# Optimization experiments

Measured on AMD Instinct MI355X. Metric: run time of the kernel, lower is better.

The kernel has to match this reference:

```python
import jax, jax.numpy as jnp
import numpy as np

B, S, D = 8, 4096, 256


def setup_inputs() -> dict:
    key = jax.random.key(0)
    kq, kk, kv, kb = jax.random.split(key, 4)
    q = jax.random.normal(kq, (B, S, D), dtype=jnp.float32)
    k = jax.random.normal(kk, (B, S, D), dtype=jnp.float32)
    v = jax.random.normal(kv, (B, S, D), dtype=jnp.float32)
    beta = jax.random.uniform(kb, (B, S), dtype=jnp.float32)
    return {"q": q, "k": k, "v": v, "beta": beta}


def reference(q, k, v, beta):
    # Delta-rule linear attention recurrence:
    #   h_t = beta_t * h_{t-1} + k_t^T v_t   (h: [B, D, D])
    #   o_t = q_t @ h_t                      (o: [B, D])
    dtype = q.dtype
    b, s, d = q.shape
    h0 = jnp.zeros((b, d, d), dtype=dtype)

    def step(h, inp):
        q_t, k_t, v_t, b_t = inp  # q_t/k_t/v_t: [B, D], b_t: [B]
        h = h * b_t[:, None, None] + jnp.einsum('bi,bj->bij', k_t, v_t)
        o_t = jnp.einsum('bi,bij->bj', q_t, h)
        return h, o_t

    xs = (q.transpose(1, 0, 2), k.transpose(1, 0, 2),
          v.transpose(1, 0, 2), beta.T)  # time-major
    _, out = jax.lax.scan(step, h0, xs)  # out: [S, B, D]
    return out.transpose(1, 0, 2)  # [B, S, D]
```

## Files before the change

### kernel.cpp

```cpp
#include <hip/hip_runtime.h>
#include <hip/hip_bf16.h>
#include <math.h>


#define B_ 8
#define S_ 4096
#define D_ 256
#define L_ 64
#define C_ (S_ / L_)
#define BC_ (B_ * C_)
#define STK 66

typedef __attribute__((ext_vector_type(8))) short s8v;
typedef __attribute__((ext_vector_type(4))) float f4v;
typedef unsigned short u16;
typedef unsigned int u32;

__device__ __forceinline__ u32 pk2(float lo, float hi) {
  union { __hip_bfloat162 h; u32 u; } cv;
  cv.h = __float22bfloat162_rn(make_float2(lo, hi));
  return cv.u;
}
__device__ __forceinline__ s8v pack8(const float4 a, const float4 b) {
  union { u32 u[4]; s8v v; } r;
  r.u[0] = pk2(a.x, a.y); r.u[1] = pk2(a.z, a.w);
  r.u[2] = pk2(b.x, b.y); r.u[3] = pk2(b.z, b.w);
  return r.v;
}

__global__ __launch_bounds__(512, 4) void ks_summary4(
    const float* __restrict__ kg, const float* __restrict__ vg,
    const float* __restrict__ beta, u16* __restrict__ A,
    float* __restrict__ P)
{
  __shared__ float ls[L_];
  __shared__ __align__(16) u16 KT[D_ * STK];
  __shared__ __align__(16) u16 VT[D_ * STK];

  const int bc = blockIdx.x;
  const int b = bc / C_, c = bc % C_;
  const int tid = threadIdx.x;
  const float* betap = beta + (size_t)b * S_ + (size_t)c * L_;
  const float* kbase = kg + ((size_t)b * S_ + (size_t)c * L_) * D_;
  const float* vbase = vg + ((size_t)b * S_ + (size_t)c * L_) * D_;

  if (tid < 64) {
    float x = log2f(fmaxf(betap[tid], 1e-30f));
#pragma unroll
    for (int off = 1; off < 64; off <<= 1) {
      float y = __shfl_up(x, off);
      if (tid >= off) x += y;
    }
    ls[tid] = x;
    if (tid == 63) P[bc] = exp2f(x);
  }
  __syncthreads();
  const float ltot = ls[63];

  {
    const int half = tid >> 8;
    const int t2 = tid & 255;
    const int iL = t2 & 7;
    const int s0 = (t2 >> 3) * 2;
    const float* src0 = (half == 0 ? kbase : vbase) + (size_t)s0 * D_;
    const float* src1 = src0 + D_;
    float w0 = 1.f, w1 = 1.f;
    if (half == 0) { w0 = exp2f(ltot - ls[s0]); w1 = exp2f(ltot - ls[s0 + 1]); }
    u16* dst = (half == 0) ? KT : VT;
#pragma unroll
    for (int p = 0; p < 8; ++p) {
      const int i0 = p * 32 + iL * 4;
      float a0[4], a1[4];
      *(float4*)a0 = *(const float4*)(src0 + i0);
      *(float4*)a1 = *(const float4*)(src1 + i0);
#pragma unroll
      for (int u = 0; u < 4; ++u)
        *(u32*)&dst[(i0 + u) * STK + s0] = pk2(a0[u] * w0, a1[u] * w1);
    }
  }
  __syncthreads();

  const int lane = tid & 63, wave = tid >> 6;
  const int quad = lane >> 4, l15 = lane & 15;
  const int i0w = wave * 32;

  s8v af[2][2];
#pragma unroll
  for (int mt = 0; mt < 2; ++mt)
#pragma unroll
    for (int ks = 0; ks < 2; ++ks)
      af[mt][ks] = *(const s8v*)&KT[(i0w + mt * 16 + l15) * STK +
                                    ks * 32 + quad * 8];
  __syncthreads();

  u16* Ab = A + (size_t)bc * D_ * D_;
  u16* BN = KT;

  for (int ng = 0; ng < 4; ++ng) {
    f4v acc[2][4];
#pragma unroll
    for (int mt = 0; mt < 2; ++mt)
#pragma unroll
      for (int nt = 0; nt < 4; ++nt) acc[mt][nt] = (f4v){0.f, 0.f, 0.f, 0.f};

#pragma unroll
    for (int ks = 0; ks < 2; ++ks) {
      const int so = ks * 32 + quad * 8;
      s8v bv[4];
#pragma unroll
      for (int nt = 0; nt < 4; ++nt)
        bv[nt] = *(const s8v*)&VT[(ng * 64 + nt * 16 + l15) * STK + so];
#pragma unroll
      for (int mt = 0; mt < 2; ++mt)
#pragma unroll
        for (int nt = 0; nt < 4; ++nt)
          acc[mt][nt] = __builtin_amdgcn_mfma_f32_16x16x32_bf16(
              af[mt][ks], bv[nt], acc[mt][nt], 0, 0, 0);
    }
#pragma unroll
    for (int mt = 0; mt < 2; ++mt)
#pragma unroll
      for (int nt = 0; nt < 4; ++nt) {
        const int jl = nt * 16 + l15;
        uint2 w;
        w.x = pk2(acc[mt][nt][0], acc[mt][nt][1]);
        w.y = pk2(acc[mt][nt][2], acc[mt][nt][3]);
        *(uint2*)&BN[jl * 264 + i0w + mt * 16 + quad * 4] = w;
      }
    __syncthreads();
    {
      const int jl = tid >> 3;
      const int il = (tid & 7) * 8;
#pragma unroll
      for (int p = 0; p < 4; ++p) {
        const int iu = il + p * 64;
        *(s8v*)&Ab[(size_t)(ng * 64 + jl) * D_ + iu] =
            *(const s8v*)&BN[jl * 264 + iu];
      }
    }
    __syncthreads();
  }
}

__global__ __launch_bounds__(256) void ks_scan4(
    u16* __restrict__ A, const float* __restrict__ P)
{
  const int g = blockIdx.x;
  const int b = g >> 7;
  const int idx = ((g & 127) << 8) + threadIdx.x;
  u16* base = A + (size_t)b * ((size_t)C_ * D_ * D_) + (size_t)idx * 2;
  const float* Pb = P + b * C_;

  float h0 = 0.f, h1 = 0.f;
  u32 cur = *(const u32*)base;
  u32 nx = *(const u32*)(base + (size_t)(D_ * D_));
  float pc = Pb[0], pn = Pb[1];
#pragma unroll 4
  for (int c = 0; c < C_; ++c) {
    u16* p = base + (size_t)c * (D_ * D_);
    u32 n2 = 0; float p2 = 0.f;
    if (c + 2 < C_) {
      n2 = *(const u32*)(p + 2 * (size_t)(D_ * D_));
      p2 = Pb[c + 2];
    }
    const float a0 = __uint_as_float(cur << 16);
    const float a1 = __uint_as_float(cur & 0xFFFF0000u);
    *(u32*)p = pk2(h0, h1);
    h0 = fmaf(pc, h0, a0);
    h1 = fmaf(pc, h1, a1);
    cur = nx; pc = pn; nx = n2; pn = p2;
  }
}

__global__ __launch_bounds__(512, 4) void ks_output4(
    const float* __restrict__ qg, const float* __restrict__ kg,
    const float* __restrict__ vg, const float* __restrict__ beta,
    const u16* __restrict__ Hg, float* __restrict__ outg)
{
  __shared__ float ls[L_];
  __shared__ float cv[L_];
  __shared__ __align__(16) u16 QB[L_ * 264];
  __shared__ __align__(16) u16 UN[L_ * 264];
  __shared__ __align__(16) u16 Tm[L_ * 72];

  const int bc = blockIdx.x;
  const int b = bc / C_, c = bc % C_;
  const int tid = threadIdx.x;
  const float* betap = beta + (size_t)b * S_ + (size_t)c * L_;
  const float* qbase = qg + ((size_t)b * S_ + (size_t)c * L_) * D_;
  const float* kbase = kg + ((size_t)b * S_ + (size_t)c * L_) * D_;
  const float* vbase = vg + ((size_t)b * S_ + (size_t)c * L_) * D_;
  const u16* Hb = Hg + (size_t)bc * D_ * D_;

  if (tid < 64) {
    float x = log2f(fmaxf(betap[tid], 1e-30f));
#pragma unroll
    for (int off = 1; off < 64; off <<= 1) {
      float y = __shfl_up(x, off);
      if (tid >= off) x += y;
    }
    ls[tid] = x;
  }

  {
    const int half = tid >> 8;
    const int t2 = tid & 255;
    const int t = t2 >> 2;
    const int cg = (t2 & 3) * 8;
    const float* src = (half == 0 ? qbase : kbase) + (size_t)t * D_ + cg;
    u16* dst = (half == 0) ? QB : UN;
#pragma unroll
    for (int p = 0; p < 8; ++p) {
      const s8v pk = pack8(*(const float4*)(src + p * 32),
                           *(const float4*)(src + p * 32 + 4));
      *(s8v*)&dst[t * 264 + cg + p * 32] = pk;
    }
  }
  __syncthreads();
  if (tid < 64) cv[tid] = exp2f(ls[tid]);

  const int lane = tid & 63, wave = tid >> 6;
  const int quad = lane >> 4, l15 = lane & 15;

  {
    const int mA = (wave & 3) * 16;
    const int nB = (wave >> 2) * 32;
    f4v accA[2];
#pragma unroll
    for (int i = 0; i < 2; ++i) accA[i] = (f4v){0.f, 0.f, 0.f, 0.f};
#pragma unroll
    for (int kd = 0; kd < 8; ++kd) {
      const int d0 = kd * 32 + quad * 8;
      const s8v af = *(const s8v*)&UN[(mA + l15) * 264 + d0];
#pragma unroll
      for (int i = 0; i < 2; ++i) {
        const s8v bf = *(const s8v*)&QB[(nB + i * 16 + l15) * 264 + d0];
        accA[i] = __builtin_amdgcn_mfma_f32_16x16x32_bf16(af, bf, accA[i],
                                                          0, 0, 0);
      }
    }
#pragma unroll
    for (int i = 0; i < 2; ++i) {
      const int t = nB + i * 16 + l15;
      const float lt = ls[t];
      const int s0 = mA + quad * 4;
      float v[4];
#pragma unroll
      for (int r = 0; r < 4; ++r) {
        const int s = s0 + r;
        v[r] = (s <= t) ? accA[i][r] * exp2f(lt - ls[s]) : 0.f;
      }
      uint2 w;
      w.x = pk2(v[0], v[1]);
      w.y = pk2(v[2], v[3]);
      *(uint2*)&Tm[t * 72 + s0] = w;
    }
  }
  __syncthreads();

  u16* VT = UN;
  {
    const int iL = tid & 15;
    const int s0 = (tid >> 4) * 2;
#pragma unroll
    for (int p = 0; p < 4; ++p) {
      const int i0 = p * 64 + iL * 4;
      float a0[4], a1[4];
      *(float4*)a0 = *(const float4*)(vbase + (size_t)s0 * D_ + i0);
      *(float4*)a1 = *(const float4*)(vbase + (size_t)(s0 + 1) * D_ + i0);
#pragma unroll
      for (int u = 0; u < 4; ++u)
        *(u32*)&VT[(i0 + u) * STK + s0] = pk2(a0[u], a1[u]);
    }
  }
  __syncthreads();

  const int j0w = wave * 32;
  f4v accS[2][4], accH[2][4];
#pragma unroll
  for (int mt = 0; mt < 2; ++mt)
#pragma unroll
    for (int nt = 0; nt < 4; ++nt) {
      accS[mt][nt] = (f4v){0.f, 0.f, 0.f, 0.f};
      accH[mt][nt] = (f4v){0.f, 0.f, 0.f, 0.f};
    }

#pragma unroll
  for (int ks = 0; ks < 2; ++ks) {
    const int so = ks * 32 + quad * 8;
    s8v af[2], bf[4];
#pragma unroll
    for (int mt = 0; mt < 2; ++mt)
      af[mt] = *(const s8v*)&VT[(j0w + mt * 16 + l15) * STK + so];
#pragma unroll
    for (int nt = 0; nt < 4; ++nt)
      bf[nt] = *(const s8v*)&Tm[(nt * 16 + l15) * 72 + so];
#pragma unroll
    for (int mt = 0; mt < 2; ++mt)
#pragma unroll
      for (int nt = 0; nt < 4; ++nt)
        accS[mt][nt] = __builtin_amdgcn_mfma_f32_16x16x32_bf16(
            af[mt], bf[nt], accS[mt][nt], 0, 0, 0);
  }

#pragma unroll
  for (int ks = 0; ks < 8; ++ks) {
    const int io = ks * 32 + quad * 8;
    s8v af[2], bf[4];
#pragma unroll
    for (int mt = 0; mt < 2; ++mt)
      af[mt] = *(const s8v*)(Hb + (size_t)(j0w + mt * 16 + l15) * D_ + io);
#pragma unroll
    for (int nt = 0; nt < 4; ++nt)
      bf[nt] = *(const s8v*)&QB[(nt * 16 + l15) * 264 + io];
#pragma unroll
    for (int mt = 0; mt < 2; ++mt)
#pragma unroll
      for (int nt = 0; nt < 4; ++nt)
        accH[mt][nt] = __builtin_amdgcn_mfma_f32_16x16x32_bf16(
            af[mt], bf[nt], accH[mt][nt], 0, 0, 0);
  }

  float* ob = outg + ((size_t)b * S_ + (size_t)c * L_) * D_;
#pragma unroll
  for (int mt = 0; mt < 2; ++mt)
#pragma unroll
    for (int nt = 0; nt < 4; ++nt) {
      const int t = nt * 16 + l15;
      const float ct = cv[t];
      const int j0 = j0w + mt * 16 + quad * 4;
      float4 o;
      o.x = accS[mt][nt][0] + ct * accH[mt][nt][0];
      o.y = accS[mt][nt][1] + ct * accH[mt][nt][1];
      o.z = accS[mt][nt][2] + ct * accH[mt][nt][2];
      o.w = accS[mt][nt][3] + ct * accH[mt][nt][3];
      *(float4*)(ob + (size_t)t * D_ + j0) = o;
    }
}

extern "C" void kernel_launch(void* const* d_in, const int* in_sizes, int n_in,
                              void* d_out, int out_size, void* d_ws,
                              size_t ws_size, hipStream_t stream) {
  const float* q = (const float*)d_in[0];
  const float* k = (const float*)d_in[1];
  const float* v = (const float*)d_in[2];
  const float* beta = (const float*)d_in[3];
  float* out = (float*)d_out;

  u16* A = (u16*)d_ws;
  float* P = (float*)((char*)d_ws + (size_t)BC_ * D_ * D_ * sizeof(u16));

  ks_summary4<<<dim3(BC_), dim3(512), 0, stream>>>(k, v, beta, A, P);
  ks_scan4<<<dim3(1024), dim3(256), 0, stream>>>(A, P);
  ks_output4<<<dim3(BC_), dim3(512), 0, stream>>>(q, k, v, beta, A, out);
}
```

Baseline: 189.7 us.

## Double chunk length to 128 to halve chunk-state traffic

```diff
diff --git a/kernel.cpp b/kernel.cpp
--- a/kernel.cpp
+++ b/kernel.cpp
@@ -6,7 +6,7 @@
 #define B_ 8
 #define S_ 4096
 #define D_ 256
-#define L_ 64
+#define L_ 128
 #define C_ (S_ / L_)
 #define BC_ (B_ * C_)
 #define STK 66
@@ -28,14 +28,35 @@
   return r.v;
 }
 
-__global__ __launch_bounds__(512, 4) void ks_summary4(
+__device__ __forceinline__ void beta_scan128(const float* betap, float* ls,
+                                             int tid) {
+  if (tid < 64) {
+    float x = log2f(fmaxf(betap[tid], 1e-30f));
+#pragma unroll
+    for (int off = 1; off < 64; off <<= 1) {
+      float y = __shfl_up(x, off);
+      if (tid >= off) x += y;
+    }
+    ls[tid] = x;
+    const float tot0 = __shfl(x, 63);
+    float z = log2f(fmaxf(betap[64 + tid], 1e-30f));
+#pragma unroll
+    for (int off = 1; off < 64; off <<= 1) {
+      float y = __shfl_up(z, off);
+      if (tid >= off) z += y;
+    }
+    ls[64 + tid] = z + tot0;
+  }
+}
+
+__global__ __launch_bounds__(512, 2) void ks_summary5(
     const float* __restrict__ kg, const float* __restrict__ vg,
     const float* __restrict__ beta, u16* __restrict__ A,
     float* __restrict__ P)
 {
   __shared__ float ls[L_];
-  __shared__ __align__(16) u16 KT[D_ * STK];
-  __shared__ __align__(16) u16 VT[D_ * STK];
+  __shared__ __align__(16) u16 U[2][256 * STK];
+  __shared__ __align__(16) u16 BN[64 * 264];
 
   const int bc = blockIdx.x;
   const int b = bc / C_, c = bc % C_;
@@ -44,38 +65,32 @@
   const float* kbase = kg + ((size_t)b * S_ + (size_t)c * L_) * D_;
   const float* vbase = vg + ((size_t)b * S_ + (size_t)c * L_) * D_;
 
-  if (tid < 64) {
-    float x = log2f(fmaxf(betap[tid], 1e-30f));
-#pragma unroll
-    for (int off = 1; off < 64; off <<= 1) {
-      float y = __shfl_up(x, off);
-      if (tid >= off) x += y;
-    }
-    ls[tid] = x;
-    if (tid == 63) P[bc] = exp2f(x);
-  }
-  __syncthreads();
-  const float ltot = ls[63];
+  beta_scan128(betap, ls, tid);
+  __syncthreads();
+  const float ltot = ls[L_ - 1];
+  if (tid == 0) P[bc] = exp2f(ltot);
+
+  const int hh = tid >> 8;
+  const int t2 = tid & 255;
+  const int iLs = t2 & 7;
+  const int s0s = (t2 >> 3) * 2;
+  const int sg = hh * 64 + s0s;
 
   {
-    const int half = tid >> 8;
-    const int t2 = tid & 255;
-    const int iL = t2 & 7;
-    const int s0 = (t2 >> 3) * 2;
-    const float* src0 = (half == 0 ? kbase : vbase) + (size_t)s0 * D_;
+    const float* src0 = kbase + (size_t)sg * D_;
     const float* src1 = src0 + D_;
-    float w0 = 1.f, w1 = 1.f;
-    if (half == 0) { w0 = exp2f(ltot - ls[s0]); w1 = exp2f(ltot - ls[s0 + 1]); }
-    u16* dst = (half == 0) ? KT : VT;
+    const float w0 = exp2f(ltot - ls[sg]);
+    const float w1 = exp2f(ltot - ls[sg + 1]);
+    u16* dst = U[hh];
 #pragma unroll
     for (int p = 0; p < 8; ++p) {
-      const int i0 = p * 32 + iL * 4;
+      const int i0 = p * 32 + iLs * 4;
       float a0[4], a1[4];
       *(float4*)a0 = *(const float4*)(src0 + i0);
       *(float4*)a1 = *(const float4*)(src1 + i0);
 #pragma unroll
       for (int u = 0; u < 4; ++u)
-        *(u32*)&dst[(i0 + u) * STK + s0] = pk2(a0[u] * w0, a1[u] * w1);
+        *(u32*)&dst[(i0 + u) * STK + s0s] = pk2(a0[u] * w0, a1[u] * w1);
     }
   }
   __syncthreads();
@@ -84,17 +99,33 @@
   const int quad = lane >> 4, l15 = lane & 15;
   const int i0w = wave * 32;
 
-  s8v af[2][2];
+  s8v af[2][4];
 #pragma unroll
   for (int mt = 0; mt < 2; ++mt)
 #pragma unroll
-    for (int ks = 0; ks < 2; ++ks)
-      af[mt][ks] = *(const s8v*)&KT[(i0w + mt * 16 + l15) * STK +
-                                    ks * 32 + quad * 8];
+    for (int ks = 0; ks < 4; ++ks)
+      af[mt][ks] = *(const s8v*)&U[ks >> 1][(i0w + mt * 16 + l15) * STK +
+                                            (ks & 1) * 32 + quad * 8];
+  __syncthreads();
+
+  {
+    const float* src0 = vbase + (size_t)sg * D_;
+    const float* src1 = src0 + D_;
+    u16* dst = U[hh];
+#pragma unroll
+    for (int p = 0; p < 8; ++p) {
+      const int i0 = p * 32 + iLs * 4;
+      float a0[4], a1[4];
+      *(float4*)a0 = *(const float4*)(src0 + i0);
+      *(float4*)a1 = *(const float4*)(src1 + i0);
+#pragma unroll
+      for (int u = 0; u < 4; ++u)
+        *(u32*)&dst[(i0 + u) * STK + s0s] = pk2(a0[u], a1[u]);
+    }
+  }
   __syncthreads();
 
   u16* Ab = A + (size_t)bc * D_ * D_;
-  u16* BN = KT;
 
   for (int ng = 0; ng < 4; ++ng) {
     f4v acc[2][4];
@@ -104,12 +135,12 @@
       for (int nt = 0; nt < 4; ++nt) acc[mt][nt] = (f4v){0.f, 0.f, 0.f, 0.f};
 
 #pragma unroll
-    for (int ks = 0; ks < 2; ++ks) {
-      const int so = ks * 32 + quad * 8;
+    for (int ks = 0; ks < 4; ++ks) {
+      const int so = (ks & 1) * 32 + quad * 8;
       s8v bv[4];
 #pragma unroll
       for (int nt = 0; nt < 4; ++nt)
-        bv[nt] = *(const s8v*)&VT[(ng * 64 + nt * 16 + l15) * STK + so];
+        bv[nt] = *(const s8v*)&U[ks >> 1][(ng * 64 + nt * 16 + l15) * STK + so];
 #pragma unroll
       for (int mt = 0; mt < 2; ++mt)
 #pragma unroll
@@ -142,7 +173,7 @@
   }
 }
 
-__global__ __launch_bounds__(256) void ks_scan4(
+__global__ __launch_bounds__(256) void ks_scan5(
     u16* __restrict__ A, const float* __restrict__ P)
 {
   const int g = blockIdx.x;
@@ -172,7 +203,7 @@
   }
 }
 
-__global__ __launch_bounds__(512, 4) void ks_output4(
+__global__ __launch_bounds__(512, 2) void ks_output5(
     const float* __restrict__ qg, const float* __restrict__ kg,
     const float* __restrict__ vg, const float* __restrict__ beta,
     const u16* __restrict__ Hg, float* __restrict__ outg)
@@ -180,8 +211,8 @@
   __shared__ float ls[L_];
   __shared__ float cv[L_];
   __shared__ __align__(16) u16 QB[L_ * 264];
-  __shared__ __align__(16) u16 UN[L_ * 264];
-  __shared__ __align__(16) u16 Tm[L_ * 72];
+  __shared__ __align__(16) u16 Tm[L_ * 136];
+  __shared__ __align__(16) u16 VT[256 * STK];
 
   const int bc = blockIdx.x;
   const int b = bc / C_, c = bc % C_;
@@ -192,148 +223,144 @@
   const float* vbase = vg + ((size_t)b * S_ + (size_t)c * L_) * D_;
   const u16* Hb = Hg + (size_t)bc * D_ * D_;
 
-  if (tid < 64) {
-    float x = log2f(fmaxf(betap[tid], 1e-30f));
-#pragma unroll
-    for (int off = 1; off < 64; off <<= 1) {
-      float y = __shfl_up(x, off);
-      if (tid >= off) x += y;
-    }
-    ls[tid] = x;
-  }
+  beta_scan128(betap, ls, tid);
 
   {
-    const int half = tid >> 8;
-    const int t2 = tid & 255;
-    const int t = t2 >> 2;
-    const int cg = (t2 & 3) * 8;
-    const float* src = (half == 0 ? qbase : kbase) + (size_t)t * D_ + cg;
-    u16* dst = (half == 0) ? QB : UN;
+    const int t = tid >> 2;
+    const int cg = (tid & 3) * 8;
+    const float* src = qbase + (size_t)t * D_ + cg;
 #pragma unroll
     for (int p = 0; p < 8; ++p) {
       const s8v pk = pack8(*(const float4*)(src + p * 32),
                            *(const float4*)(src + p * 32 + 4));
-      *(s8v*)&dst[t * 264 + cg + p * 32] = pk;
-    }
-  }
-  __syncthreads();
-  if (tid < 64) cv[tid] = exp2f(ls[tid]);
+      *(s8v*)&QB[t * 264 + cg + p * 32] = pk;
+    }
+  }
+  __syncthreads();
+  if (tid < L_) cv[tid] = exp2f(ls[tid]);
 
   const int lane = tid & 63, wave = tid >> 6;
   const int quad = lane >> 4, l15 = lane & 15;
 
   {
-    const int mA = (wave & 3) * 16;
-    const int nB = (wave >> 2) * 32;
-    f4v accA[2];
-#pragma unroll
-    for (int i = 0; i < 2; ++i) accA[i] = (f4v){0.f, 0.f, 0.f, 0.f};
+    const int mA = wave * 16;
+    f4v accA[8];
+#pragma unroll
+    for (int i = 0; i < 8; ++i) accA[i] = (f4v){0.f, 0.f, 0.f, 0.f};
 #pragma unroll
     for (int kd = 0; kd < 8; ++kd) {
       const int d0 = kd * 32 + quad * 8;
-      const s8v af = *(const s8v*)&UN[(mA + l15) * 264 + d0];
-#pragma unroll
-      for (int i = 0; i < 2; ++i) {
-        const s8v bf = *(const s8v*)&QB[(nB + i * 16 + l15) * 264 + d0];
-        accA[i] = __builtin_amdgcn_mfma_f32_16x16x32_bf16(af, bf, accA[i],
-                                                          0, 0, 0);
-      }
-    }
-#pragma unroll
-    for (int i = 0; i < 2; ++i) {
-      const int t = nB + i * 16 + l15;
+      const float* krow = kbase + (size_t)(mA + l15) * D_ + d0;
+      const s8v af = pack8(*(const float4*)krow, *(const float4*)(krow + 4));
+#pragma unroll
+      for (int nt = 0; nt < 8; ++nt) {
+        const s8v bf = *(const s8v*)&QB[(nt * 16 + l15) * 264 + d0];
+        accA[nt] = __builtin_amdgcn_mfma_f32_16x16x32_bf16(af, bf, accA[nt],
+                                                           0, 0, 0);
+      }
+    }
+#pragma unroll
+    for (int nt = 0; nt < 8; ++nt) {
+      const int t = nt * 16 + l15;
       const float lt = ls[t];
       const int s0 = mA + quad * 4;
       float v[4];
 #pragma unroll
       for (int r = 0; r < 4; ++r) {
         const int s = s0 + r;
-        v[r] = (s <= t) ? accA[i][r] * exp2f(lt - ls[s]) : 0.f;
+        v[r] = (s <= t) ? accA[nt][r] * exp2f(lt - ls[s]) : 0.f;
       }
       uint2 w;
       w.x = pk2(v[0], v[1]);
       w.y = pk2(v[2], v[3]);
-      *(uint2*)&Tm[t * 72 + s0] = w;
-    }
-  }
-  __syncthreads();
-
-  u16* VT = UN;
-  {
-    const int iL = tid & 15;
-    const int s0 = (tid >> 4) * 2;
-#pragma unroll
-    for (int p = 0; p < 4; ++p) {
-      const int i0 = p * 64 + iL * 4;
-      float a0[4], a1[4];
-      *(float4*)a0 = *(const float4*)(vbase + (size_t)s0 * D_ + i0);
-      *(float4*)a1 = *(const float4*)(vbase + (size_t)(s0 + 1) * D_ + i0);
-#pragma unroll
-      for (int u = 0; u < 4; ++u)
-        *(u32*)&VT[(i0 + u) * STK + s0] = pk2(a0[u], a1[u]);
+      *(uint2*)&Tm[t * 136 + s0] = w;
     }
   }
   __syncthreads();
 
   const int j0w = wave * 32;
-  f4v accS[2][4], accH[2][4];
+  f4v acc[2][8];
 #pragma unroll
   for (int mt = 0; mt < 2; ++mt)
 #pragma unroll
-    for (int nt = 0; nt < 4; ++nt) {
-      accS[mt][nt] = (f4v){0.f, 0.f, 0.f, 0.f};
-      accH[mt][nt] = (f4v){0.f, 0.f, 0.f, 0.f};
-    }
-
-#pragma unroll
-  for (int ks = 0; ks < 2; ++ks) {
-    const int so = ks * 32 + quad * 8;
-    s8v af[2], bf[4];
-#pragma unroll
-    for (int mt = 0; mt < 2; ++mt)
-      af[mt] = *(const s8v*)&VT[(j0w + mt * 16 + l15) * STK + so];
-#pragma unroll
-    for (int nt = 0; nt < 4; ++nt)
-      bf[nt] = *(const s8v*)&Tm[(nt * 16 + l15) * 72 + so];
-#pragma unroll
-    for (int mt = 0; mt < 2; ++mt)
-#pragma unroll
-      for (int nt = 0; nt < 4; ++nt)
-        accS[mt][nt] = __builtin_amdgcn_mfma_f32_16x16x32_bf16(
-            af[mt], bf[nt], accS[mt][nt], 0, 0, 0);
-  }
+    for (int nt = 0; nt < 8; ++nt) acc[mt][nt] = (f4v){0.f, 0.f, 0.f, 0.f};
 
 #pragma unroll
   for (int ks = 0; ks < 8; ++ks) {
     const int io = ks * 32 + quad * 8;
-    s8v af[2], bf[4];
+    s8v af[2], bf[8];
 #pragma unroll
     for (int mt = 0; mt < 2; ++mt)
       af[mt] = *(const s8v*)(Hb + (size_t)(j0w + mt * 16 + l15) * D_ + io);
 #pragma unroll
-    for (int nt = 0; nt < 4; ++nt)
+    for (int nt = 0; nt < 8; ++nt)
       bf[nt] = *(const s8v*)&QB[(nt * 16 + l15) * 264 + io];
 #pragma unroll
     for (int mt = 0; mt < 2; ++mt)
 #pragma unroll
-      for (int nt = 0; nt < 4; ++nt)
-        accH[mt][nt] = __builtin_amdgcn_mfma_f32_16x16x32_bf16(
-            af[mt], bf[nt], accH[mt][nt], 0, 0, 0);
+      for (int nt = 0; nt < 8; ++nt)
+        acc[mt][nt] = __builtin_amdgcn_mfma_f32_16x16x32_bf16(
+            af[mt], bf[nt], acc[mt][nt], 0, 0, 0);
+  }
+#pragma unroll
+  for (int nt = 0; nt < 8; ++nt) {
+    const float ct = cv[nt * 16 + l15];
+#pragma unroll
+    for (int mt = 0; mt < 2; ++mt) {
+      acc[mt][nt][0] *= ct; acc[mt][nt][1] *= ct;
+      acc[mt][nt][2] *= ct; acc[mt][nt][3] *= ct;
+    }
+  }
+
+#pragma unroll
+  for (int h = 0; h < 2; ++h) {
+    __syncthreads();
+    {
+      const int iL = tid & 15;
+      const int s0 = ((tid >> 4) & 31) * 2;
+      const float* src0 = vbase + (size_t)(h * 64 + s0) * D_;
+      const float* src1 = src0 + D_;
+#pragma unroll
+      for (int p = 0; p < 4; ++p) {
+        const int i0 = p * 64 + iL * 4;
+        float a0[4], a1[4];
+        *(float4*)a0 = *(const float4*)(src0 + i0);
+        *(float4*)a1 = *(const float4*)(src1 + i0);
+#pragma unroll
+        for (int u = 0; u < 4; ++u)
+          *(u32*)&VT[(i0 + u) * STK + s0] = pk2(a0[u], a1[u]);
+      }
+    }
+    __syncthreads();
+#pragma unroll
+    for (int ks = 0; ks < 2; ++ks) {
+      const int so = ks * 32 + quad * 8;
+      s8v af[2], bf[8];
+#pragma unroll
+      for (int mt = 0; mt < 2; ++mt)
+        af[mt] = *(const s8v*)&VT[(j0w + mt * 16 + l15) * STK + so];
+#pragma unroll
+      for (int nt = 0; nt < 8; ++nt)
+        bf[nt] = *(const s8v*)&Tm[(nt * 16 + l15) * 136 + h * 64 + so];
+#pragma unroll
+      for (int mt = 0; mt < 2; ++mt)
+#pragma unroll
+        for (int nt = 0; nt < 8; ++nt)
+          acc[mt][nt] = __builtin_amdgcn_mfma_f32_16x16x32_bf16(
+              af[mt], bf[nt], acc[mt][nt], 0, 0, 0);
+    }
   }
 
   float* ob = outg + ((size_t)b * S_ + (size_t)c * L_) * D_;
 #pragma unroll
   for (int mt = 0; mt < 2; ++mt)
 #pragma unroll
-    for (int nt = 0; nt < 4; ++nt) {
+    for (int nt = 0; nt < 8; ++nt) {
       const int t = nt * 16 + l15;
-      const float ct = cv[t];
       const int j0 = j0w + mt * 16 + quad * 4;
       float4 o;
-      o.x = accS[mt][nt][0] + ct * accH[mt][nt][0];
-      o.y = accS[mt][nt][1] + ct * accH[mt][nt][1];
-      o.z = accS[mt][nt][2] + ct * accH[mt][nt][2];
-      o.w = accS[mt][nt][3] + ct * accH[mt][nt][3];
+      o.x = acc[mt][nt][0]; o.y = acc[mt][nt][1];
+      o.z = acc[mt][nt][2]; o.w = acc[mt][nt][3];
       *(float4*)(ob + (size_t)t * D_ + j0) = o;
     }
 }
@@ -350,7 +377,7 @@
   u16* A = (u16*)d_ws;
   float* P = (float*)((char*)d_ws + (size_t)BC_ * D_ * D_ * sizeof(u16));
 
-  ks_summary4<<<dim3(BC_), dim3(512), 0, stream>>>(k, v, beta, A, P);
-  ks_scan4<<<dim3(1024), dim3(256), 0, stream>>>(A, P);
-  ks_output4<<<dim3(BC_), dim3(512), 0, stream>>>(q, k, v, beta, A, out);
-}
+  ks_summary5<<<dim3(BC_), dim3(512), 0, stream>>>(k, v, beta, A, P);
+  ks_scan5<<<dim3(1024), dim3(256), 0, stream>>>(A, P);
+  ks_output5<<<dim3(BC_), dim3(512), 0, stream>>>(q, k, v, beta, A, out);
+}
```

Result: faster. 175.5 us (-7.5%).
